# Optimization experiments

Hardware: AMD Instinct MI355X
Metric: run time of the kernel (lower is better)

Reference implementation:

```python
import jax, jax.numpy as jnp
import numpy as np

B, N, D, H = 2, 2048, 1024, 16
HD = D // H

def setup_inputs() -> dict:
    key = jax.random.key(0)
    ks = jax.random.split(key, 8)
    s = lambda fan_in: 1.0 / np.sqrt(fan_in)
    return {
        "x": jax.random.normal(ks[0], (B, N, D), jnp.float32),
        "coverage": jax.random.uniform(ks[1], (B, N, 1), jnp.float32),
        "w_qkv": jax.random.normal(ks[2], (D, 3 * D), jnp.float32) * s(D),
        "w_out": jax.random.normal(ks[3], (D, D), jnp.float32) * s(D),
        "b_out": jnp.zeros((D,), jnp.float32),
        "w_ce1": jax.random.normal(ks[4], (1, D // 4), jnp.float32),
        "b_ce1": jnp.zeros((D // 4,), jnp.float32),
        "w_ce2": jax.random.normal(ks[5], (D // 4, H), jnp.float32) * s(D // 4),
        "b_ce2": jnp.zeros((H,), jnp.float32),
        "w_fg1": jax.random.normal(ks[6], (D, D // 4), jnp.float32) * s(D),
        "b_fg1": jnp.zeros((D // 4,), jnp.float32),
        "w_fg2": jax.random.normal(ks[7], (D // 4, 1), jnp.float32) * s(D // 4),
        "b_fg2": jnp.zeros((1,), jnp.float32),
    }

def reference(x, coverage, w_qkv, w_out, b_out, w_ce1, b_ce1, w_ce2, b_ce2,
              w_fg1, b_fg1, w_fg2, b_fg2):
    b, n, d = x.shape
    h = w_ce2.shape[1]
    hd = d // h
    scale = hd ** -0.5
    qkv = x @ w_qkv  # (B,N,3D)
    q, k, v = jnp.split(qkv, 3, axis=-1)
    q = q.reshape(b, n, h, hd).transpose(0, 2, 1, 3)  # (B,H,N,hd)
    k = k.reshape(b, n, h, hd).transpose(0, 2, 1, 3)
    v = v.reshape(b, n, h, hd).transpose(0, 2, 1, 3)
    attn = jnp.einsum("bhnd,bhmd->bhnm", q, k) * scale  # (B,H,N,N)
    # coverage bias: MLP(1 -> D/4 -> H), broadcast over query dim
    cov = jax.nn.silu(coverage @ w_ce1 + b_ce1) @ w_ce2 + b_ce2  # (B,N,H)
    cov_bias = cov.transpose(0, 2, 1)[:, :, None, :]  # (B,H,1,N)
    # fusion gate on mean-pooled features
    x_pooled = x.mean(axis=1)  # (B,D)
    g = jax.nn.sigmoid(jax.nn.silu(x_pooled @ w_fg1 + b_fg1) @ w_fg2 + b_fg2)  # (B,1)
    g = g[:, :, None, None]  # (B,1,1,1)
    # g*(attn+bias) + (1-g)*attn == attn + g*bias (exact same math)
    attn = attn + g * cov_bias
    attn = jax.nn.softmax(attn, axis=-1)
    out = jnp.einsum("bhnm,bhmd->bhnd", attn, v)  # (B,H,N,hd)
    out = out.transpose(0, 2, 1, 3).reshape(b, n, d)
    return out @ w_out + b_out
```

## Files before the change

### kernel.cpp

```cpp
#include <hip/hip_runtime.h>
#include <math.h>

typedef __bf16 bf16_t;
typedef __bf16 bf16x8 __attribute__((ext_vector_type(8)));
typedef __bf16 bf16x4 __attribute__((ext_vector_type(4)));
typedef float f32x4 __attribute__((ext_vector_type(4)));

#define MFMA16(a, b, c) __builtin_amdgcn_mfma_f32_16x16x32_bf16((a), (b), (c), 0, 0, 0)

constexpr int Bc = 2, Nc = 2048, Dc = 1024, Hc = 16, HDc = 64;
constexpr float C1 = 0.18033688011112042f;
constexpr float LOG2E = 1.4426950408889634f;

__device__ __forceinline__ void glds16(const bf16_t* g, bf16_t* l) {
    __builtin_amdgcn_global_load_lds(
        (const __attribute__((address_space(1))) unsigned int*)g,
        (__attribute__((address_space(3))) unsigned int*)l, 16, 0, 0);
}

__device__ __forceinline__ void glds4(const float* g, float* l) {
    __builtin_amdgcn_global_load_lds(
        (const __attribute__((address_space(1))) unsigned int*)g,
        (__attribute__((address_space(3))) unsigned int*)l, 4, 0, 0);
}

__device__ __forceinline__ void tr64_body(const float* __restrict__ src,
                                          bf16_t* __restrict__ dst, int R, int C,
                                          int bx, int by, bf16_t* tile, int t) {
    int r0 = by * 64, c0 = bx * 64;
    int cl = t & 63, rl = t >> 6;
#pragma unroll
    for (int p = 0; p < 16; ++p) {
        int r = p * 4 + rl;
        tile[r * 66 + cl] = (bf16_t)src[(size_t)(r0 + r) * C + c0 + cl];
    }
    __syncthreads();
#pragma unroll
    for (int p = 0; p < 16; ++p) {
        int r = p * 4 + rl;
        dst[(size_t)(c0 + r) * R + r0 + cl] = tile[cl * 66 + r];
    }
}

__global__ __launch_bounds__(256) void prep(const float* __restrict__ x,
                                            bf16_t* __restrict__ Xb,
                                            const float* __restrict__ w_qkv,
                                            bf16_t* __restrict__ Wt,
                                            const float* __restrict__ w_out,
                                            bf16_t* __restrict__ WoT,
                                            float* __restrict__ pooled,
                                            const float* __restrict__ coverage,
                                            const float* __restrict__ w_ce1,
                                            const float* __restrict__ b_ce1,
                                            const float* __restrict__ w_ce2,
                                            const float* __restrict__ b_ce2,
                                            float* __restrict__ cbias) {
    __shared__ __align__(16) float smem[8768];
    int bid = blockIdx.x, t = threadIdx.x;

    if (bid < 64) {
        float* w1s = smem;
        float* b1s = smem + 256;
        float* w2s = smem + 512;
        float* part = smem + 4608;
        int b = bid >> 5, n0 = (bid & 31) * 64;
        w1s[t] = w_ce1[t];
        b1s[t] = b_ce1[t];
        {
            float4* w2v = (float4*)w2s;
            const float4* g4 = (const float4*)w_ce2;
#pragma unroll
            for (int i = 0; i < 4; ++i) w2v[i * 256 + t] = g4[i * 256 + t];
        }
        __syncthreads();
        int wv = t >> 6, lane2 = t & 63;
        float c = coverage[b * 2048 + n0 + lane2];
        float acc[16];
#pragma unroll
        for (int hh = 0; hh < 16; ++hh) acc[hh] = 0.f;
        for (int jj = 0; jj < 64; ++jj) {
            int j = wv * 64 + jj;
            float tv = fmaf(c, w1s[j], b1s[j]);
            tv = tv / (1.0f + __expf(-tv));
#pragma unroll
            for (int hh = 0; hh < 16; ++hh)
                acc[hh] = fmaf(tv, w2s[j * 16 + hh], acc[hh]);
        }
#pragma unroll
        for (int hh = 0; hh < 16; ++hh) part[lane2 * 65 + wv * 16 + hh] = acc[hh];
        __syncthreads();
#pragma unroll
        for (int i = 0; i < 4; ++i) {
            int idx = t + i * 256;
            int nl = idx >> 4, hh = idx & 15;
            const float* pr = part + nl * 65 + hh;
            float s = pr[0] + pr[16] + pr[32] + pr[48];
            cbias[((size_t)b * 16 + hh) * 2048 + n0 + nl] = LOG2E * (s + b_ce2[hh]);
        }
    } else if (bid < 320) {
        int blk = bid - 64;
        int b = blk >> 7, ch = blk & 127;
        int c = t * 4;
        float s0 = 0.f, s1 = 0.f, s2 = 0.f, s3 = 0.f;
        for (int rr = 0; rr < 16; ++rr) {
            float4 v = *(const float4*)(x + (size_t)(b * Nc + ch * 16 + rr) * Dc + c);
            s0 += v.x; s1 += v.y; s2 += v.z; s3 += v.w;
        }
        atomicAdd(&pooled[b * Dc + c + 0], s0);
        atomicAdd(&pooled[b * Dc + c + 1], s1);
        atomicAdd(&pooled[b * Dc + c + 2], s2);
        atomicAdd(&pooled[b * Dc + c + 3], s3);
    } else if (bid < 1088) {
        int bb = bid - 320;
        tr64_body(w_qkv, Wt, 1024, 3072, bb % 48, bb / 48, (bf16_t*)smem, t);
    } else if (bid < 1344) {
        int bb = bid - 1088;
        tr64_body(w_out, WoT, 1024, 1024, bb & 15, bb >> 4, (bf16_t*)smem, t);
    } else {
        int base = (bid - 1344) * 4096 + t * 4;
#pragma unroll
        for (int c = 0; c < 4; ++c) {
            int i = base + c * 1024;
            float4 v = *(const float4*)(x + i);
            bf16x4 o = { (bf16_t)v.x, (bf16_t)v.y, (bf16_t)v.z, (bf16_t)v.w };
            *(bf16x4*)(Xb + i) = o;
        }
    }
}

__global__ __launch_bounds__(256) void qkv_gemm(const bf16_t* __restrict__ Xb,
                                                const bf16_t* __restrict__ Wt,
                                                bf16_t* __restrict__ Q,
                                                bf16_t* __restrict__ Kb,
                                                bf16_t* __restrict__ Vt,
                                                const float* __restrict__ pooled,
                                                const float* __restrict__ w_fg1,
                                                const float* __restrict__ b_fg1,
                                                const float* __restrict__ w_fg2,
                                                float* __restrict__ hacc) {
    __shared__ __align__(16) bf16_t At[128 * 32];
    __shared__ __align__(16) bf16_t Bt[128 * 32];
    int t = threadIdx.x;

    if (blockIdx.y == 24) {
        __shared__ float red[4];
        int blk = blockIdx.x;
        int b = blk >> 4, jb = (blk & 15) * 16;
        for (int jj = 0; jj < 16; ++jj) {
            int j = jb + jj;
            float p = 0.f;
#pragma unroll
            for (int i = 0; i < 4; ++i) {
                int d = t * 4 + i;
                p += pooled[b * 1024 + d] * w_fg1[d * 256 + j];
            }
#pragma unroll
            for (int off = 32; off > 0; off >>= 1) p += __shfl_down(p, off);
            if ((t & 63) == 0) red[t >> 6] = p;
            __syncthreads();
            if (t == 0) {
                float hj = (red[0] + red[1] + red[2] + red[3]) * (1.0f / 2048.0f) + b_fg1[j];
                hj = hj / (1.0f + __expf(-hj));
                atomicAdd(&hacc[b], hj * w_fg2[j]);
            }
            __syncthreads();
        }
        return;
    }

    int w = t >> 6, lane = t & 63;
    int l16 = lane & 15, quad = lane >> 4;
    int wm = w & 1, wx = w >> 1;
    int m0 = blockIdx.x * 128;
    int n0 = blockIdx.y * 128;
    f32x4 acc[4][4] = {};
    int sw = (l16 >> 2) & 3;

    for (int k0 = 0; k0 < 1024; k0 += 32) {
#pragma unroll
        for (int i = 0; i < 2; ++i) {
            int fb = i * 4096 + w * 1024;
            int f = fb + lane * 16;
            int row = f >> 6;
            int ch = (f >> 4) & 3;
            int sc = ch ^ ((row >> 2) & 3);
            glds16(Wt + (size_t)(n0 + row) * 1024 + k0 + sc * 8, At + (fb >> 1));
            glds16(Xb + (size_t)(m0 + row) * 1024 + k0 + sc * 8, Bt + (fb >> 1));
        }
        __syncthreads();
        bf16x8 afr[4], bfr[4];
#pragma unroll
        for (int mi = 0; mi < 4; ++mi)
            afr[mi] = *(const bf16x8*)(At + (wm * 64 + mi * 16 + l16) * 32 + ((quad ^ sw) * 8));
#pragma unroll
        for (int ni = 0; ni < 4; ++ni)
            bfr[ni] = *(const bf16x8*)(Bt + (wx * 64 + ni * 16 + l16) * 32 + ((quad ^ sw) * 8));
#pragma unroll
        for (int mi = 0; mi < 4; ++mi)
#pragma unroll
            for (int ni = 0; ni < 4; ++ni)
                acc[mi][ni] = MFMA16(afr[mi], bfr[ni], acc[mi][ni]);
        __syncthreads();
    }

    int sec = n0 >> 10;
    float scq = (sec == 0) ? C1 : 1.0f;
#pragma unroll
    for (int mi = 0; mi < 4; ++mi) {
        int gc = n0 + wm * 64 + mi * 16 + quad * 4;
        int dcol = gc & 1023;
        int h = dcol >> 6, hd = dcol & 63;
#pragma unroll
        for (int ni = 0; ni < 4; ++ni) {
            int gx = m0 + wx * 64 + ni * 16 + l16;
            int b = gx >> 11, n = gx & 2047;
            size_t bh = (size_t)(b * 16 + h);
            if (sec == 2) {
#pragma unroll
                for (int r = 0; r < 4; ++r)
                    Vt[(bh * 64 + hd + r) * 2048 + n] = (bf16_t)acc[mi][ni][r];
            } else {
                bf16x4 pk = { (bf16_t)(acc[mi][ni][0] * scq), (bf16_t)(acc[mi][ni][1] * scq),
                              (bf16_t)(acc[mi][ni][2] * scq), (bf16_t)(acc[mi][ni][3] * scq) };
                bf16_t* dst = (sec == 0 ? Q : Kb);
                *(bf16x4*)(dst + (bh * 2048 + n) * 64 + hd) = pk;
            }
        }
    }
}

__global__ __launch_bounds__(256) void attn_k(const bf16_t* __restrict__ Q,
                                              const bf16_t* __restrict__ Kb,
                                              const bf16_t* __restrict__ Vt,
                                              const float* __restrict__ cbias,
                                              const float* __restrict__ hacc,
                                              const float* __restrict__ b_fg2,
                                              bf16_t* __restrict__ O) {
    __shared__ __align__(16) bf16_t kbuf[2][64 * 64];
    __shared__ __align__(16) bf16_t vbuf[2][64 * 64];
    __shared__ __align__(16) float bbias[2][64];
    int t = threadIdx.x, w = t >> 6, lane = t & 63;
    int l16 = lane & 15, quad = lane >> 4;
    int bh = blockIdx.y;
    int b = bh >> 4, h = bh & 15;
    int qa = blockIdx.x * 128 + w * 32;
    const bf16_t* Qh = Q + (size_t)bh * 2048 * 64;
    const bf16_t* Kh = Kb + (size_t)bh * 2048 * 64;
    const bf16_t* Vh = Vt + (size_t)bh * 64 * 2048;
    const float* bih = cbias + (size_t)bh * 2048;
    float g = 1.0f / (1.0f + __expf(-(hacc[b] + b_fg2[0])));

    int fb0 = w * 2048, fb1 = fb0 + 1024;
    int f0 = fb0 + lane * 16, f1 = fb1 + lane * 16;
    int krow0 = f0 >> 7, kch0 = ((f0 >> 4) & 7) ^ (krow0 & 7);
    int krow1 = f1 >> 7, kch1 = ((f1 >> 4) & 7) ^ (krow1 & 7);

    bf16x8 qf[2][2];
#pragma unroll
    for (int qt = 0; qt < 2; ++qt)
#pragma unroll
        for (int dh = 0; dh < 2; ++dh)
            qf[qt][dh] = *(const bf16x8*)(Qh + (size_t)(qa + qt * 16 + l16) * 64 + dh * 32 + quad * 8);

    f32x4 o[2][4] = {};
    f32x4 lacc[2] = {};
    bf16x8 onesb;
#pragma unroll
    for (int i = 0; i < 8; ++i) onesb[i] = (bf16_t)1.0f;
    int swl = l16 & 7;
    int qh = quad >> 1, ql = quad & 1;

    int bk0 = l16 * 64 + ((quad ^ swl) * 8);
    int bk1 = l16 * 64 + (((4 + quad) ^ swl) * 8);
    int bv0 = l16 * 64 + ql * 4 + ((qh ^ swl) * 8);
    int bv1 = l16 * 64 + ql * 4 + (((2 + qh) ^ swl) * 8);
    int bv2 = l16 * 64 + ql * 4 + (((4 + qh) ^ swl) * 8);
    int bv3 = l16 * 64 + ql * 4 + (((6 + qh) ^ swl) * 8);

    auto stage = [&](int tile_, int bf) {
        int jn = tile_ * 64;
        glds16(Kh + (size_t)(jn + krow0) * 64 + kch0 * 8, &kbuf[bf][fb0 >> 1]);
        glds16(Kh + (size_t)(jn + krow1) * 64 + kch1 * 8, &kbuf[bf][fb1 >> 1]);
        glds16(Vh + (size_t)krow0 * 2048 + jn + kch0 * 8, &vbuf[bf][fb0 >> 1]);
        glds16(Vh + (size_t)krow1 * 2048 + jn + kch1 * 8, &vbuf[bf][fb1 >> 1]);
        glds4(bih + jn + lane, &bbias[bf][0]);
    };

    stage(0, 0);

    for (int it = 0; it < 32; ++it) {
        int sel = it & 1;
        asm volatile("s_waitcnt lgkmcnt(0)" ::: "memory");
        __builtin_amdgcn_s_barrier();
        if (it + 1 < 32) {
            stage(it + 1, sel ^ 1);
            asm volatile("s_waitcnt vmcnt(5)" ::: "memory");
        } else {
            asm volatile("s_waitcnt vmcnt(0)" ::: "memory");
        }
        __builtin_amdgcn_s_barrier();
        __builtin_amdgcn_sched_barrier(0);

        const bf16_t* kb = &kbuf[sel][0];
        const bf16_t* vb = &vbuf[sel][0];
        const float* bp = &bbias[sel][0];

        f32x4 s[2][4];
        __builtin_amdgcn_s_setprio(1);
#pragma unroll
        for (int kt = 0; kt < 4; ++kt) {
            f32x4 bv = *(const f32x4*)(bp + kt * 16 + quad * 4);
            f32x4 bi = { bv[0] * g, bv[1] * g, bv[2] * g, bv[3] * g };
            bf16x8 kf0 = *(const bf16x8*)(kb + kt * 1024 + bk0);
            bf16x8 kf1 = *(const bf16x8*)(kb + kt * 1024 + bk1);
#pragma unroll
            for (int qt = 0; qt < 2; ++qt) {
                s[qt][kt] = MFMA16(kf0, qf[qt][0], bi);
                s[qt][kt] = MFMA16(kf1, qf[qt][1], s[qt][kt]);
            }
        }
        __builtin_amdgcn_s_setprio(0);

        bf16x8 pf[2][2];
#pragma unroll
        for (int qt = 0; qt < 2; ++qt) {
#pragma unroll
            for (int kt = 0; kt < 4; ++kt)
#pragma unroll
                for (int r = 0; r < 4; ++r)
                    s[qt][kt][r] = __builtin_amdgcn_exp2f(s[qt][kt][r]);
#pragma unroll
            for (int pv = 0; pv < 2; ++pv) {
                bf16x8 tmp;
#pragma unroll
                for (int i = 0; i < 4; ++i) {
                    tmp[i]     = (bf16_t)s[qt][2 * pv][i];
                    tmp[i + 4] = (bf16_t)s[qt][2 * pv + 1][i];
                }
                pf[qt][pv] = tmp;
            }
        }

        __builtin_amdgcn_s_setprio(1);
#pragma unroll
        for (int qt = 0; qt < 2; ++qt) {
            lacc[qt] = MFMA16(pf[qt][0], onesb, lacc[qt]);
            lacc[qt] = MFMA16(pf[qt][1], onesb, lacc[qt]);
        }
#pragma unroll
        for (int dt = 0; dt < 4; ++dt) {
            bf16x4 va0 = *(const bf16x4*)(vb + dt * 1024 + bv0);
            bf16x4 vc0 = *(const bf16x4*)(vb + dt * 1024 + bv1);
            bf16x8 vf0 = __builtin_shufflevector(va0, vc0, 0, 1, 2, 3, 4, 5, 6, 7);
            bf16x4 va1 = *(const bf16x4*)(vb + dt * 1024 + bv2);
            bf16x4 vc1 = *(const bf16x4*)(vb + dt * 1024 + bv3);
            bf16x8 vf1 = __builtin_shufflevector(va1, vc1, 0, 1, 2, 3, 4, 5, 6, 7);
#pragma unroll
            for (int qt = 0; qt < 2; ++qt) {
                o[qt][dt] = MFMA16(pf[qt][0], vf0, o[qt][dt]);
                o[qt][dt] = MFMA16(pf[qt][1], vf1, o[qt][dt]);
            }
        }
        __builtin_amdgcn_s_setprio(0);
    }

#pragma unroll
    for (int qt = 0; qt < 2; ++qt) {
        f32x4 rinv;
#pragma unroll
        for (int r = 0; r < 4; ++r) rinv[r] = 1.0f / lacc[qt][r];
#pragma unroll
        for (int dt = 0; dt < 4; ++dt)
#pragma unroll
            for (int r = 0; r < 4; ++r) {
                int row = qa + qt * 16 + quad * 4 + r;
                O[(size_t)(b * 2048 + row) * 1024 + h * 64 + dt * 16 + l16] =
                    (bf16_t)(o[qt][dt][r] * rinv[r]);
            }
    }
}

__global__ __launch_bounds__(256) void out_gemm(const bf16_t* __restrict__ A,
                                                const bf16_t* __restrict__ Wt,
                                                const float* __restrict__ bias,
                                                float* __restrict__ Cout) {
    __shared__ __align__(16) bf16_t At[128 * 32];
    __shared__ __align__(16) bf16_t Bt[128 * 32];
    int t = threadIdx.x, w = t >> 6, lane = t & 63;
    int l16 = lane & 15, quad = lane >> 4;
    int wm = w & 1, wx = w >> 1;
    int m0 = blockIdx.x * 128;
    int n0 = blockIdx.y * 128;
    f32x4 acc[4][4] = {};
    int sw = (l16 >> 2) & 3;

    for (int k0 = 0; k0 < 1024; k0 += 32) {
#pragma unroll
        for (int i = 0; i < 2; ++i) {
            int fb = i * 4096 + w * 1024;
            int f = fb + lane * 16;
            int row = f >> 6;
            int ch = (f >> 4) & 3;
            int sc = ch ^ ((row >> 2) & 3);
            glds16(Wt + (size_t)(n0 + row) * 1024 + k0 + sc * 8, At + (fb >> 1));
            glds16(A + (size_t)(m0 + row) * 1024 + k0 + sc * 8, Bt + (fb >> 1));
        }
        __syncthreads();
        bf16x8 afr[4], bfr[4];
#pragma unroll
        for (int mi = 0; mi < 4; ++mi)
            afr[mi] = *(const bf16x8*)(At + (wm * 64 + mi * 16 + l16) * 32 + ((quad ^ sw) * 8));
#pragma unroll
        for (int ni = 0; ni < 4; ++ni)
            bfr[ni] = *(const bf16x8*)(Bt + (wx * 64 + ni * 16 + l16) * 32 + ((quad ^ sw) * 8));
#pragma unroll
        for (int mi = 0; mi < 4; ++mi)
#pragma unroll
            for (int ni = 0; ni < 4; ++ni)
                acc[mi][ni] = MFMA16(afr[mi], bfr[ni], acc[mi][ni]);
        __syncthreads();
    }

#pragma unroll
    for (int mi = 0; mi < 4; ++mi) {
        int gc = n0 + wm * 64 + mi * 16 + quad * 4;
        float4 bv = *(const float4*)(bias + gc);
#pragma unroll
        for (int ni = 0; ni < 4; ++ni) {
            int gx = m0 + wx * 64 + ni * 16 + l16;
            float4 ov = { acc[mi][ni][0] + bv.x, acc[mi][ni][1] + bv.y,
                          acc[mi][ni][2] + bv.z, acc[mi][ni][3] + bv.w };
            *(float4*)(Cout + (size_t)gx * 1024 + gc) = ov;
        }
    }
}

extern "C" void kernel_launch(void* const* d_in, const int* in_sizes, int n_in,
                              void* d_out, int out_size, void* d_ws, size_t ws_size,
                              hipStream_t stream) {
    const float* x     = (const float*)d_in[0];
    const float* cov   = (const float*)d_in[1];
    const float* w_qkv = (const float*)d_in[2];
    const float* w_out = (const float*)d_in[3];
    const float* b_out = (const float*)d_in[4];
    const float* w_ce1 = (const float*)d_in[5];
    const float* b_ce1 = (const float*)d_in[6];
    const float* w_ce2 = (const float*)d_in[7];
    const float* b_ce2 = (const float*)d_in[8];
    const float* w_fg1 = (const float*)d_in[9];
    const float* b_fg1 = (const float*)d_in[10];
    const float* w_fg2 = (const float*)d_in[11];
    const float* b_fg2 = (const float*)d_in[12];

    char* ws = (char*)d_ws;
    bf16_t* Wt     = (bf16_t*)(ws);
    bf16_t* WoT    = (bf16_t*)(ws + 6291456);
    bf16_t* Xb     = (bf16_t*)(ws + 8388608);
    bf16_t* Qb     = (bf16_t*)(ws + 16777216);
    bf16_t* Kbb    = (bf16_t*)(ws + 25165824);
    bf16_t* Vt     = (bf16_t*)(ws + 33554432);
    bf16_t* Ob     = (bf16_t*)(ws + 41943040);
    float*  pooled = (float*)(ws + 50331648);
    float*  hacc   = (float*)(ws + 50339840);
    float*  biasb  = (float*)(ws + 50340096);

    hipMemsetAsync(pooled, 0, 8200, stream);
    prep<<<2368, 256, 0, stream>>>(x, Xb, w_qkv, Wt, w_out, WoT, pooled,
                                   cov, w_ce1, b_ce1, w_ce2, b_ce2, biasb);
    qkv_gemm<<<dim3(32, 25), 256, 0, stream>>>(Xb, Wt, Qb, Kbb, Vt,
                                               pooled, w_fg1, b_fg1, w_fg2, hacc);
    attn_k<<<dim3(16, 32), 256, 0, stream>>>(Qb, Kbb, Vt, biasb, hacc, b_fg2, Ob);
    out_gemm<<<dim3(32, 8), 256, 0, stream>>>(Ob, WoT, b_out, (float*)d_out);
}
```

Baseline: 240.3 us.

## Double-buffer QKV and output GEMM K-loops, preload scaled coverage bias in attention

Both the QKV and output projection GEMMs move from single-buffered LDS tiles with two __syncthreads per K step to double-buffered global_load_lds staging. The next K slice is issued before the current one is computed, using explicit waitcnt and barriers, with raised MFMA priority. The goal is to hide global-load latency behind MFMA work, at the cost of doubling LDS use per block, which may lower occupancy. The attention kernel now loads the whole per-head bias row, already multiplied by the gate g, into LDS once at start. This removes the per-iteration 4-byte global_load_lds and the per-tile multiply by g.

Measured after the change: 246.0 us. +2.4%, slower.

```diff
diff --git a/kernel.cpp b/kernel.cpp
--- a/kernel.cpp
+++ b/kernel.cpp
@@ -16,12 +16,6 @@
     __builtin_amdgcn_global_load_lds(
         (const __attribute__((address_space(1))) unsigned int*)g,
         (__attribute__((address_space(3))) unsigned int*)l, 16, 0, 0);
-}
-
-__device__ __forceinline__ void glds4(const float* g, float* l) {
-    __builtin_amdgcn_global_load_lds(
-        (const __attribute__((address_space(1))) unsigned int*)g,
-        (__attribute__((address_space(3))) unsigned int*)l, 4, 0, 0);
 }
 
 __device__ __forceinline__ void tr64_body(const float* __restrict__ src,
@@ -138,8 +132,8 @@
                                                 const float* __restrict__ b_fg1,
                                                 const float* __restrict__ w_fg2,
                                                 float* __restrict__ hacc) {
-    __shared__ __align__(16) bf16_t At[128 * 32];
-    __shared__ __align__(16) bf16_t Bt[128 * 32];
+    __shared__ __align__(16) bf16_t At[2][128 * 32];
+    __shared__ __align__(16) bf16_t Bt[2][128 * 32];
     int t = threadIdx.x;
 
     if (blockIdx.y == 24) {
@@ -176,31 +170,55 @@
     f32x4 acc[4][4] = {};
     int sw = (l16 >> 2) & 3;
 
-    for (int k0 = 0; k0 < 1024; k0 += 32) {
+    int arow[2], asc[2], aoff[2];
+#pragma unroll
+    for (int i = 0; i < 2; ++i) {
+        int fb = i * 4096 + w * 1024;
+        int f = fb + lane * 16;
+        int row = f >> 6;
+        int ch = (f >> 4) & 3;
+        arow[i] = row;
+        asc[i] = ch ^ ((row >> 2) & 3);
+        aoff[i] = fb >> 1;
+    }
+    auto stage = [&](int k0, int bf) {
 #pragma unroll
         for (int i = 0; i < 2; ++i) {
-            int fb = i * 4096 + w * 1024;
-            int f = fb + lane * 16;
-            int row = f >> 6;
-            int ch = (f >> 4) & 3;
-            int sc = ch ^ ((row >> 2) & 3);
-            glds16(Wt + (size_t)(n0 + row) * 1024 + k0 + sc * 8, At + (fb >> 1));
-            glds16(Xb + (size_t)(m0 + row) * 1024 + k0 + sc * 8, Bt + (fb >> 1));
-        }
-        __syncthreads();
+            glds16(Wt + (size_t)(n0 + arow[i]) * 1024 + k0 + asc[i] * 8, At[bf] + aoff[i]);
+            glds16(Xb + (size_t)(m0 + arow[i]) * 1024 + k0 + asc[i] * 8, Bt[bf] + aoff[i]);
+        }
+    };
+
+    stage(0, 0);
+    for (int ks = 0; ks < 32; ++ks) {
+        int sel = ks & 1;
+        asm volatile("s_waitcnt lgkmcnt(0)" ::: "memory");
+        __builtin_amdgcn_s_barrier();
+        if (ks + 1 < 32) {
+            stage((ks + 1) * 32, sel ^ 1);
+            asm volatile("s_waitcnt vmcnt(4)" ::: "memory");
+        } else {
+            asm volatile("s_waitcnt vmcnt(0)" ::: "memory");
+        }
+        __builtin_amdgcn_s_barrier();
+        __builtin_amdgcn_sched_barrier(0);
+
+        const bf16_t* Ab = At[sel];
+        const bf16_t* Bb = Bt[sel];
         bf16x8 afr[4], bfr[4];
 #pragma unroll
         for (int mi = 0; mi < 4; ++mi)
-            afr[mi] = *(const bf16x8*)(At + (wm * 64 + mi * 16 + l16) * 32 + ((quad ^ sw) * 8));
+            afr[mi] = *(const bf16x8*)(Ab + (wm * 64 + mi * 16 + l16) * 32 + ((quad ^ sw) * 8));
 #pragma unroll
         for (int ni = 0; ni < 4; ++ni)
-            bfr[ni] = *(const bf16x8*)(Bt + (wx * 64 + ni * 16 + l16) * 32 + ((quad ^ sw) * 8));
+            bfr[ni] = *(const bf16x8*)(Bb + (wx * 64 + ni * 16 + l16) * 32 + ((quad ^ sw) * 8));
+        __builtin_amdgcn_s_setprio(1);
 #pragma unroll
         for (int mi = 0; mi < 4; ++mi)
 #pragma unroll
             for (int ni = 0; ni < 4; ++ni)
                 acc[mi][ni] = MFMA16(afr[mi], bfr[ni], acc[mi][ni]);
-        __syncthreads();
+        __builtin_amdgcn_s_setprio(0);
     }
 
     int sec = n0 >> 10;
@@ -238,7 +256,7 @@
                                               bf16_t* __restrict__ O) {
     __shared__ __align__(16) bf16_t kbuf[2][64 * 64];
     __shared__ __align__(16) bf16_t vbuf[2][64 * 64];
-    __shared__ __align__(16) float bbias[2][64];
+    __shared__ __align__(16) float ball[2048];
     int t = threadIdx.x, w = t >> 6, lane = t & 63;
     int l16 = lane & 15, quad = lane >> 4;
     int bh = blockIdx.y;
@@ -250,6 +268,13 @@
     const float* bih = cbias + (size_t)bh * 2048;
     float g = 1.0f / (1.0f + __expf(-(hacc[b] + b_fg2[0])));
 
+#pragma unroll
+    for (int c = 0; c < 2; ++c) {
+        float4 v = *(const float4*)(bih + c * 1024 + t * 4);
+        float4 sv = { v.x * g, v.y * g, v.z * g, v.w * g };
+        *(float4*)(ball + c * 1024 + t * 4) = sv;
+    }
+
     int fb0 = w * 2048, fb1 = fb0 + 1024;
     int f0 = fb0 + lane * 16, f1 = fb1 + lane * 16;
     int krow0 = f0 >> 7, kch0 = ((f0 >> 4) & 7) ^ (krow0 & 7);
@@ -283,18 +308,17 @@
         glds16(Kh + (size_t)(jn + krow1) * 64 + kch1 * 8, &kbuf[bf][fb1 >> 1]);
         glds16(Vh + (size_t)krow0 * 2048 + jn + kch0 * 8, &vbuf[bf][fb0 >> 1]);
         glds16(Vh + (size_t)krow1 * 2048 + jn + kch1 * 8, &vbuf[bf][fb1 >> 1]);
-        glds4(bih + jn + lane, &bbias[bf][0]);
     };
 
     stage(0, 0);
 
     for (int it = 0; it < 32; ++it) {
-        int sel = it & 1;
+        int sel = it & 1, j0 = it * 64;
         asm volatile("s_waitcnt lgkmcnt(0)" ::: "memory");
         __builtin_amdgcn_s_barrier();
         if (it + 1 < 32) {
             stage(it + 1, sel ^ 1);
-            asm volatile("s_waitcnt vmcnt(5)" ::: "memory");
+            asm volatile("s_waitcnt vmcnt(4)" ::: "memory");
         } else {
             asm volatile("s_waitcnt vmcnt(0)" ::: "memory");
         }
@@ -303,14 +327,12 @@
 
         const bf16_t* kb = &kbuf[sel][0];
         const bf16_t* vb = &vbuf[sel][0];
-        const float* bp = &bbias[sel][0];
 
         f32x4 s[2][4];
         __builtin_amdgcn_s_setprio(1);
 #pragma unroll
         for (int kt = 0; kt < 4; ++kt) {
-            f32x4 bv = *(const f32x4*)(bp + kt * 16 + quad * 4);
-            f32x4 bi = { bv[0] * g, bv[1] * g, bv[2] * g, bv[3] * g };
+            f32x4 bi = *(const f32x4*)(ball + j0 + kt * 16 + quad * 4);
             bf16x8 kf0 = *(const bf16x8*)(kb + kt * 1024 + bk0);
             bf16x8 kf1 = *(const bf16x8*)(kb + kt * 1024 + bk1);
 #pragma unroll
@@ -384,8 +406,8 @@
                                                 const bf16_t* __restrict__ Wt,
                                                 const float* __restrict__ bias,
                                                 float* __restrict__ Cout) {
-    __shared__ __align__(16) bf16_t At[128 * 32];
-    __shared__ __align__(16) bf16_t Bt[128 * 32];
+    __shared__ __align__(16) bf16_t At[2][128 * 32];
+    __shared__ __align__(16) bf16_t Bt[2][128 * 32];
     int t = threadIdx.x, w = t >> 6, lane = t & 63;
     int l16 = lane & 15, quad = lane >> 4;
     int wm = w & 1, wx = w >> 1;
@@ -394,31 +416,55 @@
     f32x4 acc[4][4] = {};
     int sw = (l16 >> 2) & 3;
 
-    for (int k0 = 0; k0 < 1024; k0 += 32) {
+    int arow[2], asc[2], aoff[2];
+#pragma unroll
+    for (int i = 0; i < 2; ++i) {
+        int fb = i * 4096 + w * 1024;
+        int f = fb + lane * 16;
+        int row = f >> 6;
+        int ch = (f >> 4) & 3;
+        arow[i] = row;
+        asc[i] = ch ^ ((row >> 2) & 3);
+        aoff[i] = fb >> 1;
+    }
+    auto stage = [&](int k0, int bf) {
 #pragma unroll
         for (int i = 0; i < 2; ++i) {
-            int fb = i * 4096 + w * 1024;
-            int f = fb + lane * 16;
-            int row = f >> 6;
-            int ch = (f >> 4) & 3;
-            int sc = ch ^ ((row >> 2) & 3);
-            glds16(Wt + (size_t)(n0 + row) * 1024 + k0 + sc * 8, At + (fb >> 1));
-            glds16(A + (size_t)(m0 + row) * 1024 + k0 + sc * 8, Bt + (fb >> 1));
-        }
-        __syncthreads();
+            glds16(Wt + (size_t)(n0 + arow[i]) * 1024 + k0 + asc[i] * 8, At[bf] + aoff[i]);
+            glds16(A + (size_t)(m0 + arow[i]) * 1024 + k0 + asc[i] * 8, Bt[bf] + aoff[i]);
+        }
+    };
+
+    stage(0, 0);
+    for (int ks = 0; ks < 32; ++ks) {
+        int sel = ks & 1;
+        asm volatile("s_waitcnt lgkmcnt(0)" ::: "memory");
+        __builtin_amdgcn_s_barrier();
+        if (ks + 1 < 32) {
+            stage((ks + 1) * 32, sel ^ 1);
+            asm volatile("s_waitcnt vmcnt(4)" ::: "memory");
+        } else {
+            asm volatile("s_waitcnt vmcnt(0)" ::: "memory");
+        }
+        __builtin_amdgcn_s_barrier();
+        __builtin_amdgcn_sched_barrier(0);
+
+        const bf16_t* Ab = At[sel];
+        const bf16_t* Bb = Bt[sel];
         bf16x8 afr[4], bfr[4];
 #pragma unroll
         for (int mi = 0; mi < 4; ++mi)
-            afr[mi] = *(const bf16x8*)(At + (wm * 64 + mi * 16 + l16) * 32 + ((quad ^ sw) * 8));
+            afr[mi] = *(const bf16x8*)(Ab + (wm * 64 + mi * 16 + l16) * 32 + ((quad ^ sw) * 8));
 #pragma unroll
         for (int ni = 0; ni < 4; ++ni)
-            bfr[ni] = *(const bf16x8*)(Bt + (wx * 64 + ni * 16 + l16) * 32 + ((quad ^ sw) * 8));
+            bfr[ni] = *(const bf16x8*)(Bb + (wx * 64 + ni * 16 + l16) * 32 + ((quad ^ sw) * 8));
+        __builtin_amdgcn_s_setprio(1);
 #pragma unroll
         for (int mi = 0; mi < 4; ++mi)
 #pragma unroll
             for (int ni = 0; ni < 4; ++ni)
                 acc[mi][ni] = MFMA16(afr[mi], bfr[ni], acc[mi][ni]);
-        __syncthreads();
+        __builtin_amdgcn_s_setprio(0);
     }
 
 #pragma unroll
```
